# Kernel optimization log

Measured on AMD Instinct MI355X. Metric: run time of the kernel, lower is better.

## Reference

```python
import jax, jax.numpy as jnp
import numpy as np

KH, KW = 7, 7            # extraction kernel
EH, EW = 5, 5            # effective (cropped) kernel
PAD = (KH - EH) // 2     # = 1
EPS = 1e-7


def _extract_patches(x):
    # x: [B,H,W,C] -> patches [B,Ho,Wo,KH,KW,C], stride 1, VALID padding
    B, H, Wd, C = x.shape
    Ho, Wo = H - KH + 1, Wd - KW + 1
    rows = []
    for i in range(KH):
        cols = [x[:, i:i + Ho, j:j + Wo, :] for j in range(KW)]
        rows.append(jnp.stack(cols, axis=3))          # [B,Ho,Wo,KW,C]
    return jnp.stack(rows, axis=3)                     # [B,Ho,Wo,KH,KW,C]


def _rotate_bilinear(patches, angles):
    # patches: [N,KH,KW,C]; angles: [N]. Mirrors tf.contrib.image
    # angles_to_projective_transforms + transform(BILINEAR, fill=0).
    # Note: the layer's det(matrix)==0 NEAREST fallback never fires (det==1).
    N = patches.shape[0]
    c, s = jnp.cos(angles), jnp.sin(angles)
    Wm1, Hm1 = jnp.float32(KW - 1), jnp.float32(KH - 1)
    xo = (Wm1 - (c * Wm1 - s * Hm1)) * 0.5
    yo = (Hm1 - (s * Wm1 + c * Hm1)) * 0.5
    scale = jnp.float32(1.0 + EPS)   # transforms /= transforms[:,8:9]+1e-7
    a0, a1, a2 = c / scale, -s / scale, xo / scale
    a3, a4, a5 = s / scale, c / scale, yo / scale
    yg, xg = jnp.meshgrid(jnp.arange(KH, dtype=jnp.float32),
                          jnp.arange(KW, dtype=jnp.float32), indexing='ij')
    x_in = a0[:, None, None] * xg + a1[:, None, None] * yg + a2[:, None, None]
    y_in = a3[:, None, None] * xg + a4[:, None, None] * yg + a5[:, None, None]
    x0f = jnp.floor(x_in); y0f = jnp.floor(y_in)
    wx1 = x_in - x0f; wx0 = 1.0 - wx1
    wy1 = y_in - y0f; wy0 = 1.0 - wy1
    x0 = x0f.astype(jnp.int32); x1 = x0 + 1
    y0 = y0f.astype(jnp.int32); y1 = y0 + 1
    nidx = jnp.arange(N)[:, None, None]

    def corner(yi, xi, w):
        valid = ((xi >= 0) & (xi < KW) & (yi >= 0) & (yi < KH)).astype(patches.dtype)
        v = patches[nidx, jnp.clip(yi, 0, KH - 1), jnp.clip(xi, 0, KW - 1)]
        return (w * valid)[..., None] * v

    return (corner(y0, x0, wy0 * wx0) + corner(y0, x1, wy0 * wx1) +
            corner(y1, x0, wy1 * wx0) + corner(y1, x1, wy1 * wx1))


def reference(x, W, b):
    B, H, Wd, C = x.shape
    patches = _extract_patches(x)                      # [B,Ho,Wo,KH,KW,C]
    _, Ho, Wo = patches.shape[:3]
    intensity = jnp.sum(patches, axis=-1)              # [B,Ho,Wo,KH,KW]
    row_idx = jnp.repeat(jnp.arange(KH, dtype=jnp.float32), KW)   # rowMulti
    col_idx = jnp.tile(jnp.arange(KW, dtype=jnp.float32), KH)     # colMulti
    flat = intensity.reshape(-1, KH * KW)              # [N, KH*KW]
    denom = jnp.sum(flat, -1) + EPS
    cr = jnp.sum(flat * row_idx, -1) / denom - (KH - 1) / 2.0
    cc = jnp.sum(flat * col_idx, -1) / denom - (KW - 1) / 2.0
    angle = jnp.arctan2(cr, cc + EPS)                  # [N]
    patches_n = patches.reshape(-1, KH, KW, C)         # [N,KH,KW,C]
    rot = _rotate_bilinear(patches_n, angle)
    rot = rot[:, PAD:PAD + EH, PAD:PAD + EW, :]        # crop to effective
    rot = rot.reshape(B, Ho, Wo, EH * EW * C)
    w_flat = W.reshape(W.shape[0], -1)                 # [F, EH*EW*C]
    out = jnp.einsum('bhwk,fk->bhwf', rot, w_flat) + b
    return out


def setup_inputs() -> dict:
    key = jax.random.key(0)
    kx, kw, _ = jax.random.split(key, 3)
    x = jax.random.normal(kx, (8, 64, 64, 32), dtype=jnp.float32)
    W = jax.random.normal(kw, (64, EH, EW, 32), dtype=jnp.float32) * 0.05
    b = jnp.zeros((64,), dtype=jnp.float32)
    return {"x": x, "W": W, "b": b}
```

## Files before the change

### kernel.cpp

```cpp
#include <hip/hip_runtime.h>
#include <hip/hip_bf16.h>

#define EPSF 1e-7f
#define B_ 8
#define H_ 64
#define W_ 64
#define C_ 32
#define HO 58
#define WO 58
#define NF 64
#define KDIM 800

#define XTS 36
#define RS  808

typedef __bf16 v8bf __attribute__((ext_vector_type(8)));
typedef float  v4f  __attribute__((ext_vector_type(4)));

__global__ void k_wpack(const float* __restrict__ W, __bf16* __restrict__ Wp) {
    int t = blockIdx.x*256 + threadIdx.x;
    int j = t & 7; int lane = (t >> 3) & 63; int rest = t >> 9;
    int kb = rest % 25; int nt = rest / 25;
    int f = nt*16 + (lane & 15);
    int k = kb*32 + (lane >> 4)*8 + j;
    Wp[t] = (__bf16)W[f*KDIM + k];
}

__global__ __launch_bounds__(256)
void k_main(const float* __restrict__ x, const v8bf* __restrict__ Wp,
            const float* __restrict__ bias, float* __restrict__ out) {
    __shared__ float  xt[7][22][XTS];
    __shared__ __bf16 rot[16][RS];
    __shared__ float  Srow[7][22];
    __shared__ float4 pp[16];

    int tid = threadIdx.x;
    int wv = tid >> 6, lane = tid & 63;
    int m = lane & 15, q = lane >> 4;
    int wt = blockIdx.x, ho = blockIdx.y, b = blockIdx.z;
    int wo0 = wt*16;
    int npx = WO - wo0; if (npx > 16) npx = 16;
    int ncols = npx + 6;

    const float* xb = x + (size_t)((b*H_ + ho)*W_ + wo0)*C_;
    int total4 = 7*ncols*8;
    for (int e = tid; e < total4; e += 256) {
        int r = e/(ncols*8); int rem = e - r*(ncols*8);
        int c = rem >> 3;    int qq = rem & 7;
        *(float4*)&xt[r][c][qq*4] = *(const float4*)&xb[(r*W_ + c)*C_ + qq*4];
    }
    __syncthreads();

    if (tid < 7*ncols) {
        int r = tid / ncols, c = tid - r*ncols;
        float s = 0.f;
#pragma unroll
        for (int qq = 0; qq < 8; qq++) {
            float4 v = *(const float4*)&xt[r][c][qq*4];
            s += v.x + v.y + v.z + v.w;
        }
        Srow[r][c] = s;
    }
    __syncthreads();

    if (tid < npx) {
        float den = 0.f, crn = 0.f, ccn = 0.f;
#pragma unroll
        for (int i = 0; i < 7; i++)
#pragma unroll
            for (int j = 0; j < 7; j++) {
                float v = Srow[i][tid + j];
                den += v; crn += v*(float)i; ccn += v*(float)j;
            }
        float dt = den + EPSF;
        float cr = crn/dt - 3.0f;
        float cx = ccn/dt - 3.0f + EPSF;
        float r2 = cr*cr + cx*cx;
        float inv = r2 > 0.f ? rsqrtf(r2) : 0.f;
        float c = r2 > 0.f ? cx*inv : 1.0f;
        float s = cr*inv;
        const float scale = 1.0f + EPSF;
        float xo = (6.0f - (c*6.0f - s*6.0f))*0.5f;
        float yo = (6.0f - (s*6.0f + c*6.0f))*0.5f;
        pp[tid] = make_float4(c/scale, s/scale, xo/scale, yo/scale);
    }
    __syncthreads();

    for (int e = tid; e < 400; e += 256) {
        int px = e & 15; int pos = e >> 4;
        if (px < npx) {
            int py = pos/5; int yy = py + 1; int xx = pos - py*5 + 1;
            float4 p = pp[px];
            float xin = p.x*(float)xx - p.y*(float)yy + p.z;
            float yin = p.y*(float)xx + p.x*(float)yy + p.w;
            float x0f = floorf(xin), y0f = floorf(yin);
            float wx1 = xin - x0f, wx0 = 1.0f - wx1;
            float wy1 = yin - y0f, wy0 = 1.0f - wy1;
            int ix0 = (int)x0f, iy0 = (int)y0f;
            int ix1 = ix0 + 1,  iy1 = iy0 + 1;

            const float* bp[4]; float wgt[4];
            auto mkcorner = [&](int yi, int xi, float w, int idx) {
                bool valid = (xi >= 0) & (xi < 7) & (yi >= 0) & (yi < 7);
                int cy = yi < 0 ? 0 : (yi > 6 ? 6 : yi);
                int cx2 = xi < 0 ? 0 : (xi > 6 ? 6 : xi);
                bp[idx]  = &xt[cy][px + cx2][0];
                wgt[idx] = valid ? w : 0.0f;
            };
            mkcorner(iy0, ix0, wy0*wx0, 0);
            mkcorner(iy0, ix1, wy0*wx1, 1);
            mkcorner(iy1, ix0, wy1*wx0, 2);
            mkcorner(iy1, ix1, wy1*wx1, 3);

            float acc[32];
#pragma unroll
            for (int ch = 0; ch < 32; ch++) acc[ch] = 0.f;
#pragma unroll
            for (int cn = 0; cn < 4; cn++) {
                const float* src = bp[cn]; float wq = wgt[cn];
#pragma unroll
                for (int qq = 0; qq < 8; qq++) {
                    float4 v = *(const float4*)(src + qq*4);
                    acc[qq*4+0] += wq*v.x; acc[qq*4+1] += wq*v.y;
                    acc[qq*4+2] += wq*v.z; acc[qq*4+3] += wq*v.w;
                }
            }
            __bf16* dst = &rot[px][pos*32];
#pragma unroll
            for (int q8 = 0; q8 < 4; q8++) {
                v8bf o;
#pragma unroll
                for (int j = 0; j < 8; j++) o[j] = (__bf16)acc[q8*8 + j];
                *(v8bf*)&dst[q8*8] = o;
            }
        }
    }

    v8bf bfrag[25];
    {
        const v8bf* wp = Wp + (size_t)wv*25*64 + lane;
#pragma unroll
        for (int kb = 0; kb < 25; kb++) bfrag[kb] = wp[kb*64];
    }
    __syncthreads();

    v4f acc4 = {0.f, 0.f, 0.f, 0.f};
#pragma unroll
    for (int kb = 0; kb < 25; kb++) {
        v8bf a = *(const v8bf*)&rot[m][kb*32 + q*8];
        acc4 = __builtin_amdgcn_mfma_f32_16x16x32_bf16(a, bfrag[kb], acc4, 0, 0, 0);
    }
    int f = wv*16 + m;
    float bv = bias[f];
    int pixbase = (b*HO + ho)*WO + wo0;
#pragma unroll
    for (int r = 0; r < 4; r++) {
        int px = q*4 + r;
        if (px < npx) out[(size_t)(pixbase + px)*NF + f] = acc4[r] + bv;
    }
}

extern "C" void kernel_launch(void* const* d_in, const int* in_sizes, int n_in,
                              void* d_out, int out_size, void* d_ws, size_t ws_size,
                              hipStream_t stream) {
    const float* x    = (const float*)d_in[0];
    const float* W    = (const float*)d_in[1];
    const float* bias = (const float*)d_in[2];
    float* out = (float*)d_out;
    __bf16* Wp = (__bf16*)d_ws;

    k_wpack<<<dim3(200), 256, 0, stream>>>(W, Wp);
    k_main<<<dim3(4, HO, B_), 256, 0, stream>>>(x, (const v8bf*)Wp, bias, out);
}
```

Before: 83.46 us.

## Stage input tile as bf16, fuse load with row sums, split weight loads

Each thread now loads its input column straight from global memory, computes the channel row-sum in registers, and writes a bf16 copy into shared memory. This removes the separate float staging pass and one barrier, and halves the shared-memory footprint. The bilinear interpolation unpacks bf16 pairs with shifts. Weight fragments are loaded in two halves so the second half overlaps the first MFMAs, and a launch-bounds occupancy hint of 4 is added. The input is now quantized to bf16 before interpolation rather than after, which adds rounding error, and the 16-column index path assumes ncols==16 for the last tile.

```diff
diff --git a/kernel.cpp b/kernel.cpp
--- a/kernel.cpp
+++ b/kernel.cpp
@@ -11,7 +11,7 @@
 #define NF 64
 #define KDIM 800
 
-#define XTS 36
+#define XBS 40
 #define RS  808
 
 typedef __bf16 v8bf __attribute__((ext_vector_type(8)));
@@ -26,10 +26,10 @@
     Wp[t] = (__bf16)W[f*KDIM + k];
 }
 
-__global__ __launch_bounds__(256)
+__global__ __launch_bounds__(256, 4)
 void k_main(const float* __restrict__ x, const v8bf* __restrict__ Wp,
             const float* __restrict__ bias, float* __restrict__ out) {
-    __shared__ float  xt[7][22][XTS];
+    __shared__ __bf16 xtb[7][22][XBS];
     __shared__ __bf16 rot[16][RS];
     __shared__ float  Srow[7][22];
     __shared__ float4 pp[16];
@@ -42,24 +42,29 @@
     int npx = WO - wo0; if (npx > 16) npx = 16;
     int ncols = npx + 6;
 
-    const float* xb = x + (size_t)((b*H_ + ho)*W_ + wo0)*C_;
-    int total4 = 7*ncols*8;
-    for (int e = tid; e < total4; e += 256) {
-        int r = e/(ncols*8); int rem = e - r*(ncols*8);
-        int c = rem >> 3;    int qq = rem & 7;
-        *(float4*)&xt[r][c][qq*4] = *(const float4*)&xb[(r*W_ + c)*C_ + qq*4];
-    }
-    __syncthreads();
+    float bv = bias[wv*16 + m];
 
     if (tid < 7*ncols) {
-        int r = tid / ncols, c = tid - r*ncols;
+        int r, c;
+        if (ncols == 22) { r = tid/22; c = tid - r*22; }
+        else             { r = tid >> 4; c = tid & 15; }
+        const float* src = x + (size_t)((b*H_ + ho + r)*W_ + wo0 + c)*C_;
+        float4 vq[8];
+#pragma unroll
+        for (int qq = 0; qq < 8; qq++) vq[qq] = *(const float4*)(src + qq*4);
         float s = 0.f;
 #pragma unroll
-        for (int qq = 0; qq < 8; qq++) {
-            float4 v = *(const float4*)&xt[r][c][qq*4];
-            s += v.x + v.y + v.z + v.w;
+        for (int qq = 0; qq < 8; qq++) s += vq[qq].x + vq[qq].y + vq[qq].z + vq[qq].w;
+        Srow[r][c] = s;
+#pragma unroll
+        for (int h8 = 0; h8 < 4; h8++) {
+            v8bf o;
+            o[0]=(__bf16)vq[h8*2].x;   o[1]=(__bf16)vq[h8*2].y;
+            o[2]=(__bf16)vq[h8*2].z;   o[3]=(__bf16)vq[h8*2].w;
+            o[4]=(__bf16)vq[h8*2+1].x; o[5]=(__bf16)vq[h8*2+1].y;
+            o[6]=(__bf16)vq[h8*2+1].z; o[7]=(__bf16)vq[h8*2+1].w;
+            *(v8bf*)&xtb[r][c][h8*8] = o;
         }
-        Srow[r][c] = s;
     }
     __syncthreads();
 
@@ -99,12 +104,12 @@
             int ix0 = (int)x0f, iy0 = (int)y0f;
             int ix1 = ix0 + 1,  iy1 = iy0 + 1;
 
-            const float* bp[4]; float wgt[4];
+            const __bf16* bp[4]; float wgt[4];
             auto mkcorner = [&](int yi, int xi, float w, int idx) {
                 bool valid = (xi >= 0) & (xi < 7) & (yi >= 0) & (yi < 7);
                 int cy = yi < 0 ? 0 : (yi > 6 ? 6 : yi);
                 int cx2 = xi < 0 ? 0 : (xi > 6 ? 6 : xi);
-                bp[idx]  = &xt[cy][px + cx2][0];
+                bp[idx]  = &xtb[cy][px + cx2][0];
                 wgt[idx] = valid ? w : 0.0f;
             };
             mkcorner(iy0, ix0, wy0*wx0, 0);
@@ -112,17 +117,23 @@
             mkcorner(iy1, ix0, wy1*wx0, 2);
             mkcorner(iy1, ix1, wy1*wx1, 3);
 
-            float acc[32];
+            float accx[16], accy[16];
 #pragma unroll
-            for (int ch = 0; ch < 32; ch++) acc[ch] = 0.f;
+            for (int i = 0; i < 16; i++) { accx[i] = 0.f; accy[i] = 0.f; }
 #pragma unroll
             for (int cn = 0; cn < 4; cn++) {
-                const float* src = bp[cn]; float wq = wgt[cn];
+                const __bf16* src = bp[cn]; float wq = wgt[cn];
 #pragma unroll
-                for (int qq = 0; qq < 8; qq++) {
-                    float4 v = *(const float4*)(src + qq*4);
-                    acc[qq*4+0] += wq*v.x; acc[qq*4+1] += wq*v.y;
-                    acc[qq*4+2] += wq*v.z; acc[qq*4+3] += wq*v.w;
+                for (int q8 = 0; q8 < 4; q8++) {
+                    union { v8bf v; unsigned u[4]; } uv;
+                    uv.v = *(const v8bf*)(src + q8*8);
+#pragma unroll
+                    for (int j = 0; j < 4; j++) {
+                        float lo = __uint_as_float(uv.u[j] << 16);
+                        float hi = __uint_as_float(uv.u[j] & 0xffff0000u);
+                        accx[q8*4+j] += wq*lo;
+                        accy[q8*4+j] += wq*hi;
+                    }
                 }
             }
             __bf16* dst = &rot[px][pos*32];
@@ -130,28 +141,37 @@
             for (int q8 = 0; q8 < 4; q8++) {
                 v8bf o;
 #pragma unroll
-                for (int j = 0; j < 8; j++) o[j] = (__bf16)acc[q8*8 + j];
-                *(v8bf*)&dst[q8*8] = o;
+                for (int j = 0; j < 4; j++) {
+                    o[2*j]   = (__bf16)accx[q8*4+j];
+                    o[2*j+1] = (__bf16)accy[q8*4+j];
+                }
+                *(v8bf*)&rot[px][pos*32 + q8*8] = o;
             }
+            (void)dst;
         }
     }
 
-    v8bf bfrag[25];
-    {
-        const v8bf* wp = Wp + (size_t)wv*25*64 + lane;
+    const v8bf* wp = Wp + (size_t)wv*25*64 + lane;
+    v8bf bfA[13];
 #pragma unroll
-        for (int kb = 0; kb < 25; kb++) bfrag[kb] = wp[kb*64];
-    }
+    for (int kb = 0; kb < 13; kb++) bfA[kb] = wp[kb*64];
     __syncthreads();
 
     v4f acc4 = {0.f, 0.f, 0.f, 0.f};
+    v8bf bfB[12];
 #pragma unroll
-    for (int kb = 0; kb < 25; kb++) {
+    for (int kb = 0; kb < 12; kb++) bfB[kb] = wp[(13 + kb)*64];
+#pragma unroll
+    for (int kb = 0; kb < 13; kb++) {
         v8bf a = *(const v8bf*)&rot[m][kb*32 + q*8];
-        acc4 = __builtin_amdgcn_mfma_f32_16x16x32_bf16(a, bfrag[kb], acc4, 0, 0, 0);
+        acc4 = __builtin_amdgcn_mfma_f32_16x16x32_bf16(a, bfA[kb], acc4, 0, 0, 0);
+    }
+#pragma unroll
+    for (int kb = 0; kb < 12; kb++) {
+        v8bf a = *(const v8bf*)&rot[m][(13 + kb)*32 + q*8];
+        acc4 = __builtin_amdgcn_mfma_f32_16x16x32_bf16(a, bfB[kb], acc4, 0, 0, 0);
     }
     int f = wv*16 + m;
-    float bv = bias[f];
     int pixbase = (b*HO + ho)*WO + wo0;
 #pragma unroll
     for (int r = 0; r < 4; r++) {
```

Result: faster. 78.88 us (-5.5%).
